# Optimization experiments

Measured on AMD Instinct MI355X. Metric: run time of the kernel, lower is better.

## Reference

```python
import jax, jax.numpy as jnp
import numpy as np

B, T, D, H = 4, 2048, 1024, 16
HD = D // H  # 64

def setup_inputs() -> dict:
    key = jax.random.key(0)
    k1, k2, k3 = jax.random.split(key, 3)
    scale = 1.0 / np.sqrt(D)
    x = jax.random.normal(k1, (B, T, D), dtype=jnp.float32)
    w_qkv = jax.random.normal(k2, (D, 3 * D), dtype=jnp.float32) * scale
    w_o = jax.random.normal(k3, (D, D), dtype=jnp.float32) * scale
    return {"x": x, "w_qkv": w_qkv, "w_o": w_o}

def reference(x, w_qkv, w_o):
    b, t, d = x.shape
    qkv = jnp.einsum('btd,de->bte', x, w_qkv)  # [B,T,3D]
    q, k, v = jnp.split(qkv, 3, axis=-1)
    # [B,H,T,hd]
    q = q.reshape(b, t, H, HD).transpose(0, 2, 1, 3)
    k = k.reshape(b, t, H, HD).transpose(0, 2, 1, 3)
    v = v.reshape(b, t, H, HD).transpose(0, 2, 1, 3)
    scores = jnp.einsum('bhqd,bhkd->bhqk', q, k) * (1.0 / jnp.sqrt(jnp.asarray(HD, x.dtype)))
    causal = jnp.tril(jnp.ones((t, t), dtype=bool))
    scores = jnp.where(causal[None, None, :, :], scores, -jnp.inf)
    weights = jax.nn.softmax(scores, axis=-1)
    out = jnp.einsum('bhqk,bhkd->bhqd', weights, v)
    out = out.transpose(0, 2, 1, 3).reshape(b, t, d)
    return jnp.einsum('btd,de->bte', out, w_o)
```

## Files before the change

kernel.cpp:

```cpp
#include <hip/hip_runtime.h>
#include <hip/hip_bf16.h>
#include <stdint.h>

#define HD 64
#define NH 16
#define TT 2048
#define DD 1024

typedef uint16_t u16;
typedef __bf16 bf16_t;
typedef bf16_t bf16x8 __attribute__((ext_vector_type(8)));
typedef float f32x4 __attribute__((ext_vector_type(4)));

__device__ __forceinline__ u16 f2b(float f) {
    union { float f; uint32_t u; } v; v.f = f;
    uint32_t u = v.u;
    u += 0x7fff + ((u >> 16) & 1);
    return (u16)(u >> 16);
}

__device__ __forceinline__ u16 b16(float f) {
    union { __bf16 h; u16 u; } c; c.h = (__bf16)f; return c.u;
}

__device__ __forceinline__ void gload16(const void* g, void* l) {
    __builtin_amdgcn_global_load_lds(
        (__attribute__((address_space(1))) void*)g,
        (__attribute__((address_space(3))) void*)l, 16, 0, 0);
}


__global__ void f32_to_bf16_vec(const float* __restrict__ in, u16* __restrict__ out, int n4) {
    int i = blockIdx.x * 256 + threadIdx.x;
    if (i >= n4) return;
    float4 v = ((const float4*)in)[i];
    ushort4 r;
    r.x = f2b(v.x); r.y = f2b(v.y); r.z = f2b(v.z); r.w = f2b(v.w);
    ((ushort4*)out)[i] = r;
}

__global__ void transpose_f32_bf16(const float* __restrict__ in, u16* __restrict__ out, int R, int C) {
    __shared__ float tile[32][33];
    const int tx = threadIdx.x, ty = threadIdx.y;
    const int c0 = blockIdx.x * 32, r0 = blockIdx.y * 32;
#pragma unroll
    for (int j = 0; j < 32; j += 8)
        tile[ty + j][tx] = in[(size_t)(r0 + ty + j) * C + c0 + tx];
    __syncthreads();
#pragma unroll
    for (int j = 0; j < 32; j += 8)
        out[(size_t)(c0 + ty + j) * R + r0 + tx] = f2b(tile[tx][ty + j]);
}


template<int MODE>
__global__ __launch_bounds__(512, 2)
void gemm256(const u16* __restrict__ A, const u16* __restrict__ Bt,
             int N, int K,
             u16* __restrict__ oq, u16* __restrict__ ok, u16* __restrict__ ovT,
             float* __restrict__ of)
{
    __shared__ __align__(16) u16 As[3][128 * 64];
    __shared__ __align__(16) u16 Bs[3][256 * 64];
    const int tid = threadIdx.x;
    const int lane = tid & 63, l15 = lane & 15, g = lane >> 4;
    const int wid = tid >> 6, wm = wid >> 2, wn = wid & 3;

    const int gx = gridDim.x;
    const int nwg = gx * gridDim.y;
    const int wgid = blockIdx.y * gx + blockIdx.x;
    const int cpx = nwg >> 3;
    const int sid = (wgid & 7) * cpx + (wgid >> 3);
    const long row0 = (long)(sid / gx) * 128;
    const long col0 = (long)(sid % gx) * 256;

    const u16* Ag = A + row0 * K;
    const u16* Bg = Bt + col0 * K;

    const f32x4 z4 = {0.f, 0.f, 0.f, 0.f};
    f32x4 acc[4][4];
#pragma unroll
    for (int i = 0; i < 4; i++)
#pragma unroll
        for (int n = 0; n < 4; n++) acc[i][n] = z4;

    const int swz = l15 & 7;

#define STG(t_, s_) do {                                                                                    \
        const int ko = (t_) << 6;                                                                           \
        { const int c = tid;        const int r_ = c >> 3;                                                  \
          gload16(Ag + (size_t)r_ * K + ko + (((c & 7) ^ (r_ & 7)) << 3), &As[s_][c << 3]); }               \
        { const int c = tid + 512;  const int r_ = c >> 3;                                                  \
          gload16(Ag + (size_t)r_ * K + ko + (((c & 7) ^ (r_ & 7)) << 3), &As[s_][c << 3]); }               \
        { const int c = tid;        const int r_ = c >> 3;                                                  \
          gload16(Bg + (size_t)r_ * K + ko + (((c & 7) ^ (r_ & 7)) << 3), &Bs[s_][c << 3]); }               \
        { const int c = tid + 512;  const int r_ = c >> 3;                                                  \
          gload16(Bg + (size_t)r_ * K + ko + (((c & 7) ^ (r_ & 7)) << 3), &Bs[s_][c << 3]); }               \
        { const int c = tid + 1024; const int r_ = c >> 3;                                                  \
          gload16(Bg + (size_t)r_ * K + ko + (((c & 7) ^ (r_ & 7)) << 3), &Bs[s_][c << 3]); }               \
        { const int c = tid + 1536; const int r_ = c >> 3;                                                  \
          gload16(Bg + (size_t)r_ * K + ko + (((c & 7) ^ (r_ & 7)) << 3), &Bs[s_][c << 3]); }               \
    } while (0)

    const int NT = K >> 6;
    STG(0, 0);
    STG(1, 1);
    int scur = 0;
    for (int t = 0; t < NT; ++t) {
        if (t + 1 < NT) asm volatile("s_waitcnt vmcnt(6)" ::: "memory");
        else            asm volatile("s_waitcnt vmcnt(0)" ::: "memory");
        __builtin_amdgcn_s_barrier();
        const int sstg = (scur == 0) ? 2 : scur - 1;
        if (t + 2 < NT) STG(t + 2, sstg);

        bf16x8 a0[4], b0[4], a1[4], b1[4];
        const int p0 = (g ^ swz) << 3, p1 = ((g ^ swz) ^ 4) << 3;
#pragma unroll
        for (int m = 0; m < 4; m++) {
            const int rA = (wm * 64 + m * 16 + l15) * 64;
            a0[m] = *(const bf16x8*)&As[scur][rA + p0];
            a1[m] = *(const bf16x8*)&As[scur][rA + p1];
        }
#pragma unroll
        for (int n = 0; n < 4; n++) {
            const int rB = (wn * 64 + n * 16 + l15) * 64;
            b0[n] = *(const bf16x8*)&Bs[scur][rB + p0];
            b1[n] = *(const bf16x8*)&Bs[scur][rB + p1];
        }
        __builtin_amdgcn_s_setprio(1);
#pragma unroll
        for (int m = 0; m < 4; m++)
#pragma unroll
            for (int n = 0; n < 4; n++)
                acc[m][n] = __builtin_amdgcn_mfma_f32_16x16x32_bf16(a0[m], b0[n], acc[m][n], 0, 0, 0);
#pragma unroll
        for (int m = 0; m < 4; m++)
#pragma unroll
            for (int n = 0; n < 4; n++)
                acc[m][n] = __builtin_amdgcn_mfma_f32_16x16x32_bf16(a1[m], b1[n], acc[m][n], 0, 0, 0);
        __builtin_amdgcn_s_setprio(0);
        scur = (scur == 2) ? 0 : scur + 1;
    }
#undef STG

    if (MODE == 0) {
        const int which = (int)(col0 >> 10);
        const long b = row0 >> 11;
#pragma unroll
        for (int m = 0; m < 4; m++) {
            const long r = row0 + wm * 64 + m * 16 + g * 4;
            const long t = r & (TT - 1);
#pragma unroll
            for (int n = 0; n < 4; n++) {
                const long c = col0 + wn * 64 + n * 16 + l15;
                const int h  = (int)((c >> 6) & 15);
                const int hd = (int)(c & 63);
                if (which == 0) {
#pragma unroll
                    for (int e = 0; e < 4; e++)
                        oq[((b * NH + h) * TT + t + e) * HD + hd] = f2b(acc[m][n][e] * 0.125f);
                } else if (which == 1) {
#pragma unroll
                    for (int e = 0; e < 4; e++)
                        ok[((b * NH + h) * TT + t + e) * HD + hd] = f2b(acc[m][n][e]);
                } else {
                    ushort4 pk;
                    pk.x = f2b(acc[m][n][0]); pk.y = f2b(acc[m][n][1]);
                    pk.z = f2b(acc[m][n][2]); pk.w = f2b(acc[m][n][3]);
                    *(ushort4*)&ovT[((b * NH + h) * HD + hd) * TT + t] = pk;
                }
            }
        }
    } else {
#pragma unroll
        for (int m = 0; m < 4; m++) {
            const long r = row0 + wm * 64 + m * 16 + g * 4;
#pragma unroll
            for (int n = 0; n < 4; n++) {
                const long c = col0 + wn * 64 + n * 16 + l15;
#pragma unroll
                for (int e = 0; e < 4; e++)
                    of[(r + e) * (long)N + c] = acc[m][n][e];
            }
        }
    }
}


__global__ __launch_bounds__(256, 3)
void attn_fwd(const u16* __restrict__ gq, const u16* __restrict__ gk,
              const u16* __restrict__ gvT, u16* __restrict__ o)
{
    __shared__ __align__(16) u16 Klds[2][64 * 64];
    __shared__ __align__(16) u16 Vlds[2][64 * 64];
    __shared__ __align__(16) u16 Plds[4][32 * 64];

    const int tid = threadIdx.x;
    const int wv = tid >> 6, lane = tid & 63, l15 = lane & 15, g = lane >> 4;
    const int bh = blockIdx.x & 63;
    const int qt = 15 - (blockIdx.x >> 6);
    const int q0 = qt * 128;
    const int qw0 = q0 + wv * 32;

    const u16* qbase = gq + (size_t)bh * TT * HD;
    const u16* kbase = gk + (size_t)bh * TT * HD;
    const u16* vbase = gvT + (size_t)bh * HD * TT;

    const float NEG_INF = -__builtin_inff();
    const f32x4 z4 = {0.f, 0.f, 0.f, 0.f};

    bf16x8 qf[2][2];
#pragma unroll
    for (int qi = 0; qi < 2; qi++)
#pragma unroll
        for (int hs = 0; hs < 2; hs++)
            qf[qi][hs] = *(const bf16x8*)(qbase + (size_t)(qw0 + qi * 16 + l15) * HD + hs * 32 + g * 8);

    f32x4 o_acc[2][4];
    float m[2], ls[2];
#pragma unroll
    for (int qi = 0; qi < 2; qi++) {
#pragma unroll
        for (int n = 0; n < 4; n++) o_acc[qi][n] = z4;
        m[qi] = NEG_INF; ls[qi] = 0.f;
    }

    const int r0_ = tid >> 3, c0_ = tid & 7;
    const int r1_ = (tid + 256) >> 3, c1_ = (tid + 256) & 7;

#define STAGE(buf, k0s)                                                                    \
    do {                                                                                   \
        gload16(kbase + (size_t)((k0s) + r0_) * HD + ((c0_ ^ (r0_ & 7)) * 8), &Klds[buf][tid * 8]);          \
        gload16(kbase + (size_t)((k0s) + r1_) * HD + ((c1_ ^ (r1_ & 7)) * 8), &Klds[buf][(tid + 256) * 8]);  \
        gload16(vbase + (size_t)r0_ * TT + (k0s) + ((c0_ ^ (r0_ & 7)) * 8), &Vlds[buf][tid * 8]);            \
        gload16(vbase + (size_t)r1_ * TT + (k0s) + ((c1_ ^ (r1_ & 7)) * 8), &Vlds[buf][(tid + 256) * 8]);    \
    } while (0)

    const int nkt = q0 / 64 + 2;
    STAGE(0, 0);
    for (int kt = 0; kt < nkt; ++kt) {
        const int k0 = kt * 64;
        const int cur = kt & 1;
        if (kt + 1 < nkt) {
            STAGE(cur ^ 1, k0 + 64);
            asm volatile("s_waitcnt vmcnt(4)" ::: "memory");
        } else {
            asm volatile("s_waitcnt vmcnt(0)" ::: "memory");
        }
        __builtin_amdgcn_s_barrier();
        if (k0 <= qw0 + 31) {
            const int sw = l15 & 7;
            f32x4 s2[2][4];
            __builtin_amdgcn_s_setprio(1);
#pragma unroll
            for (int kb = 0; kb < 4; kb++) {
                bf16x8 kf0 = *(const bf16x8*)&Klds[cur][(kb * 16 + l15) * 64 + ((g ^ sw) * 8)];
                bf16x8 kf1 = *(const bf16x8*)&Klds[cur][(kb * 16 + l15) * 64 + (((4 + g) ^ sw) * 8)];
#pragma unroll
                for (int qi = 0; qi < 2; qi++) {
                    f32x4 t0 = __builtin_amdgcn_mfma_f32_16x16x32_bf16(kf0, qf[qi][0], z4, 0, 0, 0);
                    s2[qi][kb] = __builtin_amdgcn_mfma_f32_16x16x32_bf16(kf1, qf[qi][1], t0, 0, 0, 0);
                }
            }
            __builtin_amdgcn_s_setprio(0);
            if (k0 + 63 > qw0) {
#pragma unroll
                for (int qi = 0; qi < 2; qi++)
#pragma unroll
                    for (int kb = 0; kb < 4; kb++)
#pragma unroll
                        for (int e = 0; e < 4; e++) {
                            const int kk = k0 + kb * 16 + g * 4 + e;
                            const int qq = qw0 + qi * 16 + l15;
                            if (kk > qq) s2[qi][kb][e] = NEG_INF;
                        }
            }
#pragma unroll
            for (int qi = 0; qi < 2; qi++) {
                f32x4 mx = s2[qi][0];
#pragma unroll
                for (int kb = 1; kb < 4; kb++)
#pragma unroll
                    for (int e = 0; e < 4; e++) mx[e] = fmaxf(mx[e], s2[qi][kb][e]);
                float pmax = fmaxf(fmaxf(mx[0], mx[1]), fmaxf(mx[2], mx[3]));
                pmax = fmaxf(pmax, __shfl_xor(pmax, 16));
                pmax = fmaxf(pmax, __shfl_xor(pmax, 32));
                float mn = m[qi];
                const int resc = !__all(pmax <= mn + 8.f);
                if (resc) {
                    const float mold = mn;
                    mn = fmaxf(mold, pmax);
                    m[qi] = mn;
                    const float sc = __expf(mold - mn);
                    ls[qi] *= sc;
#pragma unroll
                    for (int e = 0; e < 4; e++) {
                        const float sce = __shfl(sc, (lane & 48) + (((lane >> 4) & 3) << 2) + e);
#pragma unroll
                        for (int n = 0; n < 4; n++) o_acc[qi][n][e] *= sce;
                    }
                }
                const int prow = qi * 16 + l15;
                u16* pb = &Plds[wv][prow * 64];
                float rsum = 0.f;
#pragma unroll
                for (int kb = 0; kb < 4; kb++) {
                    const float p0 = __expf(s2[qi][kb][0] - mn);
                    const float p1 = __expf(s2[qi][kb][1] - mn);
                    const float p2 = __expf(s2[qi][kb][2] - mn);
                    const float p3 = __expf(s2[qi][kb][3] - mn);
                    rsum += (p0 + p1) + (p2 + p3);
                    ushort4 pk;
                    pk.x = b16(p0); pk.y = b16(p1); pk.z = b16(p2); pk.w = b16(p3);
                    *(ushort4*)&pb[(((kb << 2) + g) ^ l15) * 4] = pk;
                }
                rsum += __shfl_xor(rsum, 16);
                rsum += __shfl_xor(rsum, 32);
                ls[qi] += rsum;
            }
#pragma unroll
            for (int ks = 0; ks < 2; ks++) {
                bf16x8 vf[4];
#pragma unroll
                for (int n = 0; n < 4; n++)
                    vf[n] = *(const bf16x8*)&Vlds[cur][(n * 16 + l15) * 64 + (((ks * 4 + g) ^ sw) * 8)];
                __builtin_amdgcn_s_setprio(1);
#pragma unroll
                for (int qi = 0; qi < 2; qi++) {
                    const u16* pb = &Plds[wv][(qi * 16 + l15) * 64];
                    const int G0 = ((ks << 3) + (g << 1)) ^ l15;
                    const int G1 = ((ks << 3) + (g << 1) + 1) ^ l15;
                    const uint2 ra = *(const uint2*)&pb[G0 * 4];
                    const uint2 rb = *(const uint2*)&pb[G1 * 4];
                    union { uint32_t w[4]; bf16x8 v; } pu;
                    pu.w[0] = ra.x; pu.w[1] = ra.y; pu.w[2] = rb.x; pu.w[3] = rb.y;
#pragma unroll
                    for (int n = 0; n < 4; n++)
                        o_acc[qi][n] = __builtin_amdgcn_mfma_f32_16x16x32_bf16(pu.v, vf[n], o_acc[qi][n], 0, 0, 0);
                }
                __builtin_amdgcn_s_setprio(0);
            }
        }
        __builtin_amdgcn_s_barrier();
    }
#undef STAGE

    const int b = bh >> 4, h = bh & 15;
#pragma unroll
    for (int qi = 0; qi < 2; qi++) {
        const float linv = 1.f / ls[qi];
#pragma unroll
        for (int e = 0; e < 4; e++) {
            const float inv = __shfl(linv, (lane & 48) + (((lane >> 4) & 3) << 2) + e);
            const int t = qw0 + qi * 16 + g * 4 + e;
#pragma unroll
            for (int n = 0; n < 4; n++)
                o[((size_t)(b * TT + t)) * DD + h * HD + n * 16 + l15] = f2b(o_acc[qi][n][e] * inv);
        }
    }
}


extern "C" void kernel_launch(void* const* d_in, const int* in_sizes, int n_in,
                              void* d_out, int out_size, void* d_ws, size_t ws_size,
                              hipStream_t stream)
{
    const float* x     = (const float*)d_in[0];
    const float* w_qkv = (const float*)d_in[1];
    const float* w_o   = (const float*)d_in[2];
    float* out = (float*)d_out;
    char* ws = (char*)d_ws;

    u16* xb    = (u16*)(ws);
    u16* wqkvT = (u16*)(ws + 16777216);
    u16* woT   = (u16*)(ws + 23068672);
    u16* wsq   = (u16*)(ws + 25165824);
    u16* wsk   = (u16*)(ws + 41943040);
    u16* wsvT  = (u16*)(ws + 58720256);
    u16* attno = (u16*)(ws + 75497472);

    f32_to_bf16_vec<<<8192, 256, 0, stream>>>(x, xb, 2097152);
    dim3 tb(32, 8);
    transpose_f32_bf16<<<dim3(96, 32), tb, 0, stream>>>(w_qkv, wqkvT, 1024, 3072);
    transpose_f32_bf16<<<dim3(32, 32), tb, 0, stream>>>(w_o,   woT,   1024, 1024);

    gemm256<0><<<dim3(12, 64), 512, 0, stream>>>(xb, wqkvT, 3072, 1024, wsq, wsk, wsvT, nullptr);
    attn_fwd<<<1024, 256, 0, stream>>>(wsq, wsk, wsvT, attno);
    gemm256<1><<<dim3(4, 64), 512, 0, stream>>>(attno, woT, 1024, 1024, nullptr, nullptr, nullptr, out);
}
```

Before: 179.3 us.

## Restructure GEMM into half-K phased pipeline with 256x128 tiles and XCD mapping

The GEMM tile changes from 128x256 to 256x128, with a 4x2 wave layout. The 1-D grid is now mapped so each XCD gets a contiguous column band. Each K-step of the main loop is split into two halves, each with its own LDS fragment loads, a partial global prefetch, barriers and an MFMA burst at raised priority. This interleaves the memory and matrix work more finely across waves. The cost is extra barriers and sched_barrier fences, which may limit the compiler's freedom to overlap work.

```diff
diff --git a/kernel.cpp b/kernel.cpp
--- a/kernel.cpp
+++ b/kernel.cpp
@@ -55,24 +55,21 @@
 
 template<int MODE>
 __global__ __launch_bounds__(512, 2)
-void gemm256(const u16* __restrict__ A, const u16* __restrict__ Bt,
-             int N, int K,
-             u16* __restrict__ oq, u16* __restrict__ ok, u16* __restrict__ ovT,
-             float* __restrict__ of)
+void gemm8p(const u16* __restrict__ A, const u16* __restrict__ Bt,
+            int N, int K,
+            u16* __restrict__ oq, u16* __restrict__ ok, u16* __restrict__ ovT,
+            float* __restrict__ of)
 {
-    __shared__ __align__(16) u16 As[3][128 * 64];
-    __shared__ __align__(16) u16 Bs[3][256 * 64];
+    __shared__ __align__(16) u16 As[3][256 * 64];
+    __shared__ __align__(16) u16 Bs[3][128 * 64];
     const int tid = threadIdx.x;
     const int lane = tid & 63, l15 = lane & 15, g = lane >> 4;
-    const int wid = tid >> 6, wm = wid >> 2, wn = wid & 3;
-
-    const int gx = gridDim.x;
-    const int nwg = gx * gridDim.y;
-    const int wgid = blockIdx.y * gx + blockIdx.x;
-    const int cpx = nwg >> 3;
-    const int sid = (wgid & 7) * cpx + (wgid >> 3);
-    const long row0 = (long)(sid / gx) * 128;
-    const long col0 = (long)(sid % gx) * 256;
+    const int wid = tid >> 6, wm = wid >> 1, wn = wid & 1;
+
+    const int gx = N >> 7, cx = gx >> 3;
+    const int j = blockIdx.x >> 3, xcd = blockIdx.x & 7;
+    const long col0 = (long)(xcd * cx + (j >> 5)) * 128;
+    const long row0 = (long)(j & 31) * 256;
 
     const u16* Ag = A + row0 * K;
     const u16* Bg = Bt + col0 * K;
@@ -86,62 +83,78 @@
 
     const int swz = l15 & 7;
 
-#define STG(t_, s_) do {                                                                                    \
-        const int ko = (t_) << 6;                                                                           \
-        { const int c = tid;        const int r_ = c >> 3;                                                  \
-          gload16(Ag + (size_t)r_ * K + ko + (((c & 7) ^ (r_ & 7)) << 3), &As[s_][c << 3]); }               \
-        { const int c = tid + 512;  const int r_ = c >> 3;                                                  \
-          gload16(Ag + (size_t)r_ * K + ko + (((c & 7) ^ (r_ & 7)) << 3), &As[s_][c << 3]); }               \
-        { const int c = tid;        const int r_ = c >> 3;                                                  \
-          gload16(Bg + (size_t)r_ * K + ko + (((c & 7) ^ (r_ & 7)) << 3), &Bs[s_][c << 3]); }               \
-        { const int c = tid + 512;  const int r_ = c >> 3;                                                  \
-          gload16(Bg + (size_t)r_ * K + ko + (((c & 7) ^ (r_ & 7)) << 3), &Bs[s_][c << 3]); }               \
-        { const int c = tid + 1024; const int r_ = c >> 3;                                                  \
-          gload16(Bg + (size_t)r_ * K + ko + (((c & 7) ^ (r_ & 7)) << 3), &Bs[s_][c << 3]); }               \
-        { const int c = tid + 1536; const int r_ = c >> 3;                                                  \
-          gload16(Bg + (size_t)r_ * K + ko + (((c & 7) ^ (r_ & 7)) << 3), &Bs[s_][c << 3]); }               \
+#define STG1(t_, s_) do { const int ko = (t_) << 6;                                               \
+        { const int c = tid;        const int r_ = c >> 3;                                        \
+          gload16(Ag + (size_t)r_ * K + ko + (((c & 7) ^ (r_ & 7)) << 3), &As[s_][c << 3]); }     \
+        { const int c = tid + 512;  const int r_ = c >> 3;                                        \
+          gload16(Ag + (size_t)r_ * K + ko + (((c & 7) ^ (r_ & 7)) << 3), &As[s_][c << 3]); }     \
+        { const int c = tid;        const int r_ = c >> 3;                                        \
+          gload16(Bg + (size_t)r_ * K + ko + (((c & 7) ^ (r_ & 7)) << 3), &Bs[s_][c << 3]); }     \
     } while (0)
+#define STG2(t_, s_) do { const int ko = (t_) << 6;                                               \
+        { const int c = tid + 1024; const int r_ = c >> 3;                                        \
+          gload16(Ag + (size_t)r_ * K + ko + (((c & 7) ^ (r_ & 7)) << 3), &As[s_][c << 3]); }     \
+        { const int c = tid + 1536; const int r_ = c >> 3;                                        \
+          gload16(Ag + (size_t)r_ * K + ko + (((c & 7) ^ (r_ & 7)) << 3), &As[s_][c << 3]); }     \
+        { const int c = tid + 512;  const int r_ = c >> 3;                                        \
+          gload16(Bg + (size_t)r_ * K + ko + (((c & 7) ^ (r_ & 7)) << 3), &Bs[s_][c << 3]); }     \
+    } while (0)
 
     const int NT = K >> 6;
-    STG(0, 0);
-    STG(1, 1);
-    int scur = 0;
+    STG1(0, 0); STG2(0, 0);
+    STG1(1, 1); STG2(1, 1);
+    asm volatile("s_waitcnt vmcnt(6)" ::: "memory");
+    __builtin_amdgcn_s_barrier();
+
+    int sc = 0;
     for (int t = 0; t < NT; ++t) {
-        if (t + 1 < NT) asm volatile("s_waitcnt vmcnt(6)" ::: "memory");
-        else            asm volatile("s_waitcnt vmcnt(0)" ::: "memory");
-        __builtin_amdgcn_s_barrier();
-        const int sstg = (scur == 0) ? 2 : scur - 1;
-        if (t + 2 < NT) STG(t + 2, sstg);
-
-        bf16x8 a0[4], b0[4], a1[4], b1[4];
-        const int p0 = (g ^ swz) << 3, p1 = ((g ^ swz) ^ 4) << 3;
-#pragma unroll
-        for (int m = 0; m < 4; m++) {
-            const int rA = (wm * 64 + m * 16 + l15) * 64;
-            a0[m] = *(const bf16x8*)&As[scur][rA + p0];
-            a1[m] = *(const bf16x8*)&As[scur][rA + p1];
-        }
-#pragma unroll
-        for (int n = 0; n < 4; n++) {
-            const int rB = (wn * 64 + n * 16 + l15) * 64;
-            b0[n] = *(const bf16x8*)&Bs[scur][rB + p0];
-            b1[n] = *(const bf16x8*)&Bs[scur][rB + p1];
-        }
+        const int sn = (sc == 0) ? 2 : sc - 1;
+        bf16x8 a0[4], b0[4];
+#pragma unroll
+        for (int m = 0; m < 4; m++)
+            a0[m] = *(const bf16x8*)&As[sc][(wm * 64 + m * 16 + l15) * 64 + ((g ^ swz) << 3)];
+#pragma unroll
+        for (int n = 0; n < 4; n++)
+            b0[n] = *(const bf16x8*)&Bs[sc][(wn * 64 + n * 16 + l15) * 64 + ((g ^ swz) << 3)];
+        if (t + 2 < NT) STG1(t + 2, sn);
+        __builtin_amdgcn_s_barrier();
+        asm volatile("s_waitcnt lgkmcnt(0)" ::: "memory");
+        __builtin_amdgcn_sched_barrier(0);
         __builtin_amdgcn_s_setprio(1);
 #pragma unroll
         for (int m = 0; m < 4; m++)
 #pragma unroll
             for (int n = 0; n < 4; n++)
                 acc[m][n] = __builtin_amdgcn_mfma_f32_16x16x32_bf16(a0[m], b0[n], acc[m][n], 0, 0, 0);
+        __builtin_amdgcn_s_setprio(0);
+        __builtin_amdgcn_s_barrier();
+        bf16x8 a1[4], b1[4];
+#pragma unroll
+        for (int m = 0; m < 4; m++)
+            a1[m] = *(const bf16x8*)&As[sc][(wm * 64 + m * 16 + l15) * 64 + (((4 + g) ^ swz) << 3)];
+#pragma unroll
+        for (int n = 0; n < 4; n++)
+            b1[n] = *(const bf16x8*)&Bs[sc][(wn * 64 + n * 16 + l15) * 64 + (((4 + g) ^ swz) << 3)];
+        if (t + 2 < NT) STG2(t + 2, sn);
+        __builtin_amdgcn_s_barrier();
+        asm volatile("s_waitcnt lgkmcnt(0)" ::: "memory");
+        __builtin_amdgcn_sched_barrier(0);
+        __builtin_amdgcn_s_setprio(1);
 #pragma unroll
         for (int m = 0; m < 4; m++)
 #pragma unroll
             for (int n = 0; n < 4; n++)
                 acc[m][n] = __builtin_amdgcn_mfma_f32_16x16x32_bf16(a1[m], b1[n], acc[m][n], 0, 0, 0);
         __builtin_amdgcn_s_setprio(0);
-        scur = (scur == 2) ? 0 : scur + 1;
+        if (t + 1 < NT) {
+            if (t + 2 < NT) asm volatile("s_waitcnt vmcnt(6)" ::: "memory");
+            else            asm volatile("s_waitcnt vmcnt(0)" ::: "memory");
+        }
+        __builtin_amdgcn_s_barrier();
+        sc = (sc == 2) ? 0 : sc + 1;
     }
-#undef STG
+#undef STG1
+#undef STG2
 
     if (MODE == 0) {
         const int which = (int)(col0 >> 10);
@@ -384,7 +397,7 @@
     transpose_f32_bf16<<<dim3(96, 32), tb, 0, stream>>>(w_qkv, wqkvT, 1024, 3072);
     transpose_f32_bf16<<<dim3(32, 32), tb, 0, stream>>>(w_o,   woT,   1024, 1024);
 
-    gemm256<0><<<dim3(12, 64), 512, 0, stream>>>(xb, wqkvT, 3072, 1024, wsq, wsk, wsvT, nullptr);
+    gemm8p<0><<<768, 512, 0, stream>>>(xb, wqkvT, 3072, 1024, wsq, wsk, wsvT, nullptr);
     attn_fwd<<<1024, 256, 0, stream>>>(wsq, wsk, wsvT, attno);
-    gemm256<1><<<dim3(4, 64), 512, 0, stream>>>(attno, woT, 1024, 1024, nullptr, nullptr, nullptr, out);
-}
+    gemm8p<1><<<256, 512, 0, stream>>>(attno, woT, 1024, 1024, nullptr, nullptr, nullptr, out);
+}
```

Result: slower. 183.0 us (+2.1%).

## Reshape GEMM tiles to 256x128 with K-step 32 and higher occupancy

Applied to the files above, without the earlier changes.

Both projection GEMMs change from 128x256 output tiles with a K-step of 64 to 256x128 tiles with a K-step of 32. Shared memory per block halves, and the launch bound asks for 4 blocks per CU instead of 2, aiming to raise occupancy and latency hiding. The LDS XOR swizzle is reworked for 32-wide rows, and fragment loads now happen before the next stage's prefetch is issued. Each iteration does half the MFMA work per barrier, so synchronization overhead per unit of work doubles. Asking for 8 waves per SIMD may force heavy register spilling, since the 64-float accumulator alone fills the per-wave budget.

```diff
diff --git a/kernel.cpp b/kernel.cpp
--- a/kernel.cpp
+++ b/kernel.cpp
@@ -54,25 +54,23 @@
 
 
 template<int MODE>
-__global__ __launch_bounds__(512, 2)
-void gemm256(const u16* __restrict__ A, const u16* __restrict__ Bt,
-             int N, int K,
-             u16* __restrict__ oq, u16* __restrict__ ok, u16* __restrict__ ovT,
-             float* __restrict__ of)
+__global__ __launch_bounds__(512, 4)
+void gemm9(const u16* __restrict__ A, const u16* __restrict__ Bt,
+           int N, int K, int nwg,
+           u16* __restrict__ oq, u16* __restrict__ ok, u16* __restrict__ ovT,
+           float* __restrict__ of)
 {
-    __shared__ __align__(16) u16 As[3][128 * 64];
-    __shared__ __align__(16) u16 Bs[3][256 * 64];
+    __shared__ __align__(16) u16 As[3][256 * 32];
+    __shared__ __align__(16) u16 Bs[3][128 * 32];
     const int tid = threadIdx.x;
     const int lane = tid & 63, l15 = lane & 15, g = lane >> 4;
-    const int wid = tid >> 6, wm = wid >> 2, wn = wid & 3;
-
-    const int gx = gridDim.x;
-    const int nwg = gx * gridDim.y;
-    const int wgid = blockIdx.y * gx + blockIdx.x;
+    const int wid = tid >> 6, wm = wid >> 1, wn = wid & 1;
+
+    const int gx = N >> 7;
     const int cpx = nwg >> 3;
-    const int sid = (wgid & 7) * cpx + (wgid >> 3);
-    const long row0 = (long)(sid / gx) * 128;
-    const long col0 = (long)(sid % gx) * 256;
+    const int sid = (blockIdx.x & 7) * cpx + (blockIdx.x >> 3);
+    const long row0 = (long)(sid / gx) * 256;
+    const long col0 = (long)(sid % gx) * 128;
 
     const u16* Ag = A + row0 * K;
     const u16* Bg = Bt + col0 * K;
@@ -84,62 +82,42 @@
 #pragma unroll
         for (int n = 0; n < 4; n++) acc[i][n] = z4;
 
-    const int swz = l15 & 7;
-
-#define STG(t_, s_) do {                                                                                    \
-        const int ko = (t_) << 6;                                                                           \
-        { const int c = tid;        const int r_ = c >> 3;                                                  \
-          gload16(Ag + (size_t)r_ * K + ko + (((c & 7) ^ (r_ & 7)) << 3), &As[s_][c << 3]); }               \
-        { const int c = tid + 512;  const int r_ = c >> 3;                                                  \
-          gload16(Ag + (size_t)r_ * K + ko + (((c & 7) ^ (r_ & 7)) << 3), &As[s_][c << 3]); }               \
-        { const int c = tid;        const int r_ = c >> 3;                                                  \
-          gload16(Bg + (size_t)r_ * K + ko + (((c & 7) ^ (r_ & 7)) << 3), &Bs[s_][c << 3]); }               \
-        { const int c = tid + 512;  const int r_ = c >> 3;                                                  \
-          gload16(Bg + (size_t)r_ * K + ko + (((c & 7) ^ (r_ & 7)) << 3), &Bs[s_][c << 3]); }               \
-        { const int c = tid + 1024; const int r_ = c >> 3;                                                  \
-          gload16(Bg + (size_t)r_ * K + ko + (((c & 7) ^ (r_ & 7)) << 3), &Bs[s_][c << 3]); }               \
-        { const int c = tid + 1536; const int r_ = c >> 3;                                                  \
-          gload16(Bg + (size_t)r_ * K + ko + (((c & 7) ^ (r_ & 7)) << 3), &Bs[s_][c << 3]); }               \
+    const int swz = (l15 >> 1) & 3;
+
+#define STG(t_, s_) do { const int ko = (t_) << 5;                                                 \
+        { const int c = tid;       const int r_ = c >> 2;                                          \
+          gload16(Ag + (size_t)r_ * K + ko + ((((c & 3) ^ ((r_ >> 1) & 3))) << 3), &As[s_][c << 3]); } \
+        { const int c = tid + 512; const int r_ = c >> 2;                                          \
+          gload16(Ag + (size_t)r_ * K + ko + ((((c & 3) ^ ((r_ >> 1) & 3))) << 3), &As[s_][c << 3]); } \
+        { const int c = tid;       const int r_ = c >> 2;                                          \
+          gload16(Bg + (size_t)r_ * K + ko + ((((c & 3) ^ ((r_ >> 1) & 3))) << 3), &Bs[s_][c << 3]); } \
     } while (0)
 
-    const int NT = K >> 6;
+    const int NT = K >> 5;
     STG(0, 0);
     STG(1, 1);
-    int scur = 0;
+    int sc = 0;
     for (int t = 0; t < NT; ++t) {
-        if (t + 1 < NT) asm volatile("s_waitcnt vmcnt(6)" ::: "memory");
+        if (t < NT - 1) asm volatile("s_waitcnt vmcnt(3)" ::: "memory");
         else            asm volatile("s_waitcnt vmcnt(0)" ::: "memory");
         __builtin_amdgcn_s_barrier();
-        const int sstg = (scur == 0) ? 2 : scur - 1;
-        if (t + 2 < NT) STG(t + 2, sstg);
-
-        bf16x8 a0[4], b0[4], a1[4], b1[4];
-        const int p0 = (g ^ swz) << 3, p1 = ((g ^ swz) ^ 4) << 3;
-#pragma unroll
-        for (int m = 0; m < 4; m++) {
-            const int rA = (wm * 64 + m * 16 + l15) * 64;
-            a0[m] = *(const bf16x8*)&As[scur][rA + p0];
-            a1[m] = *(const bf16x8*)&As[scur][rA + p1];
-        }
-#pragma unroll
-        for (int n = 0; n < 4; n++) {
-            const int rB = (wn * 64 + n * 16 + l15) * 64;
-            b0[n] = *(const bf16x8*)&Bs[scur][rB + p0];
-            b1[n] = *(const bf16x8*)&Bs[scur][rB + p1];
-        }
+        bf16x8 af[4], bfr[4];
+#pragma unroll
+        for (int m = 0; m < 4; m++)
+            af[m]  = *(const bf16x8*)&As[sc][(wm * 64 + m * 16 + l15) * 32 + ((g ^ swz) << 3)];
+#pragma unroll
+        for (int n = 0; n < 4; n++)
+            bfr[n] = *(const bf16x8*)&Bs[sc][(wn * 64 + n * 16 + l15) * 32 + ((g ^ swz) << 3)];
+        const int sn = (sc == 0) ? 2 : sc - 1;
+        if (t + 2 < NT) STG(t + 2, sn);
         __builtin_amdgcn_s_setprio(1);
 #pragma unroll
         for (int m = 0; m < 4; m++)
 #pragma unroll
             for (int n = 0; n < 4; n++)
-                acc[m][n] = __builtin_amdgcn_mfma_f32_16x16x32_bf16(a0[m], b0[n], acc[m][n], 0, 0, 0);
-#pragma unroll
-        for (int m = 0; m < 4; m++)
-#pragma unroll
-            for (int n = 0; n < 4; n++)
-                acc[m][n] = __builtin_amdgcn_mfma_f32_16x16x32_bf16(a1[m], b1[n], acc[m][n], 0, 0, 0);
+                acc[m][n] = __builtin_amdgcn_mfma_f32_16x16x32_bf16(af[m], bfr[n], acc[m][n], 0, 0, 0);
         __builtin_amdgcn_s_setprio(0);
-        scur = (scur == 2) ? 0 : scur + 1;
+        sc = (sc == 2) ? 0 : sc + 1;
     }
 #undef STG
 
@@ -384,7 +362,7 @@
     transpose_f32_bf16<<<dim3(96, 32), tb, 0, stream>>>(w_qkv, wqkvT, 1024, 3072);
     transpose_f32_bf16<<<dim3(32, 32), tb, 0, stream>>>(w_o,   woT,   1024, 1024);
 
-    gemm256<0><<<dim3(12, 64), 512, 0, stream>>>(xb, wqkvT, 3072, 1024, wsq, wsk, wsvT, nullptr);
+    gemm9<0><<<768, 512, 0, stream>>>(xb, wqkvT, 3072, 1024, 768, wsq, wsk, wsvT, nullptr);
     attn_fwd<<<1024, 256, 0, stream>>>(wsq, wsk, wsvT, attno);
-    gemm256<1><<<dim3(4, 64), 512, 0, stream>>>(attno, woT, 1024, 1024, nullptr, nullptr, nullptr, out);
-}
+    gemm9<1><<<256, 512, 0, stream>>>(attno, woT, 1024, 1024, 256, nullptr, nullptr, nullptr, out);
+}
```

New measurement: 164.3 us. 1.09x faster.
